# Optimization experiments

Measured on AMD Instinct MI355X. Metric: run time of the kernel, lower is better.

## Reference

```python
import jax, jax.numpy as jnp
import numpy as np

B, T, C, H = 2, 2048, 1024, 16
D = C // H
SCALE = D ** -0.5


def setup_inputs() -> dict:
    key = jax.random.key(0)
    ks = jax.random.split(key, 13)
    s = 0.02
    return {
        "hidden_states": jax.random.normal(ks[0], (B, T, C), dtype=jnp.float32),
        "Wq": jax.random.normal(ks[1], (C, C), dtype=jnp.float32) * s,
        "bq": jax.random.normal(ks[2], (C,), dtype=jnp.float32) * s,
        "Wk": jax.random.normal(ks[3], (C, C), dtype=jnp.float32) * s,
        "bk": jax.random.normal(ks[4], (C,), dtype=jnp.float32) * s,
        "Wv": jax.random.normal(ks[5], (C, C), dtype=jnp.float32) * s,
        "bv": jax.random.normal(ks[6], (C,), dtype=jnp.float32) * s,
        "Wo": jax.random.normal(ks[7], (C, C), dtype=jnp.float32) * s,
        "bo": jax.random.normal(ks[8], (C,), dtype=jnp.float32) * s,
        "Wr1": jax.random.normal(ks[9], (C, C), dtype=jnp.float32) * s,
        "br1": jax.random.normal(ks[10], (C,), dtype=jnp.float32) * s,
        "Wr2": jax.random.normal(ks[11], (C, 3), dtype=jnp.float32) * s,
        "br2": jax.random.normal(ks[12], (3,), dtype=jnp.float32) * s,
    }


def _heads(x):  # [B,T,C] -> [B,H,T,D]
    return x.reshape(B, T, H, D).transpose(0, 2, 1, 3)


def reference(hidden_states, Wq, bq, Wk, bk, Wv, bv, Wo, bo, Wr1, br1, Wr2, br2):
    x = hidden_states
    q = _heads(x @ Wq + bq)  # [B,H,T,D]

    # three memory levels: full sequence, mean-pooled (broadcast), all-zero
    L1 = x
    L2 = jnp.broadcast_to(jnp.mean(x, axis=1, keepdims=True), (B, T, C))
    L3 = jnp.zeros_like(x)

    # soft routing gate per token over the 3 levels
    routing = jax.nn.softmax(jnp.tanh(x @ Wr1 + br1) @ Wr2 + br2, axis=-1)  # [B,T,3]

    out = jnp.zeros_like(x)
    for i, mem in enumerate((L1, L2, L3)):
        k = _heads(mem @ Wk + bk)  # [B,H,T,D]
        v = _heads(mem @ Wv + bv)
        scores = jnp.einsum('bhqd,bhkd->bhqk', q, k) * SCALE
        probs = jax.nn.softmax(scores, axis=-1)
        mo = jnp.einsum('bhqk,bhkd->bhqd', probs, v)  # [B,H,T,D]
        mo = mo.transpose(0, 2, 1, 3).reshape(B, T, C) @ Wo + bo
        out = out + routing[:, :, i:i + 1] * mo
    return out
```

## Files before the change

### kernel.cpp

```cpp
#include <hip/hip_runtime.h>
#include <hip/hip_bf16.h>
#include <math.h>

#define Bdim 2
#define Tdim 2048
#define Cdim 1024
#define Hdim 16
#define SCALE 0.125f
#define M_TOT (Bdim * Tdim)
#define Kdim Cdim
#define KVB 64

typedef __attribute__((ext_vector_type(8))) short bf16x8;
typedef __attribute__((ext_vector_type(4))) float f32x4;
typedef unsigned short ushort_t;

union U8 { bf16x8 v; ushort4 u4[2]; };

__device__ __forceinline__ unsigned short f2bf(float f) {
    union { float f; unsigned u; } v; v.f = f;
    unsigned r = (v.u + 0x7FFFu + ((v.u >> 16) & 1u)) >> 16;
    return (unsigned short)r;
}
__device__ __forceinline__ float bf2f(unsigned short h) {
    union { unsigned u; float f; } v; v.u = ((unsigned)h) << 16;
    return v.f;
}

template <int CTRL>
__device__ __forceinline__ float dppf(float v) {
    int r = __builtin_amdgcn_update_dpp(0, __builtin_bit_cast(int, v), CTRL, 0xF, 0xF, false);
    return __builtin_bit_cast(float, r);
}
__device__ __forceinline__ float rmax16(float v) {
    v = fmaxf(v, dppf<0xB1>(v));
    v = fmaxf(v, dppf<0x4E>(v));
    v = fmaxf(v, dppf<0x124>(v));
    v = fmaxf(v, dppf<0x128>(v));
    return v;
}
__device__ __forceinline__ float rsum16(float v) {
    v += dppf<0xB1>(v);
    v += dppf<0x4E>(v);
    v += dppf<0x124>(v);
    v += dppf<0x128>(v);
    return v;
}

__global__ void colmean_kernel(const float* __restrict__ x, float* __restrict__ m) {
    int b = blockIdx.x;
    int c = blockIdx.y * 256 + threadIdx.x;
    int t0 = blockIdx.z * 64;
    float s = 0.f;
    for (int t = t0; t < t0 + 64; ++t)
        s += x[((size_t)b * Tdim + t) * Cdim + c];
    atomicAdd(&m[b * Cdim + c], s * (1.0f / Tdim));
}

__global__ void biasinit_kernel(const float* __restrict__ bias, float* __restrict__ out, int R) {
    int c = blockIdx.x * 256 + threadIdx.x;
    for (int r = 0; r < R; ++r) out[(size_t)r * Cdim + c] = bias[c];
}

__global__ void gemv3_part_kernel(const float* __restrict__ rows, const float* __restrict__ W,
                                  float* __restrict__ out) {
    int c = blockIdx.x * 256 + threadIdx.x;
    int r = blockIdx.y;
    int k0 = blockIdx.z * 128;
    const float* rp = rows + (size_t)r * Cdim;
    float s = 0.f;
    for (int k = k0; k < k0 + 128; ++k)
        s += rp[k] * W[(size_t)k * Cdim + c];
    atomicAdd(&out[(size_t)r * Cdim + c], s);
}

__global__ void cast_bf16_kernel(const float* __restrict__ in, ushort_t* __restrict__ out) {
    int i = blockIdx.x * 256 + threadIdx.x;
    float4 v = ((const float4*)in)[i];
    ushort4 o;
    o.x = f2bf(v.x); o.y = f2bf(v.y); o.z = f2bf(v.z); o.w = f2bf(v.w);
    ((ushort4*)out)[i] = o;
}

__global__ __launch_bounds__(256) void transpose_cast_kernel(const float* __restrict__ W,
                                                             ushort_t* __restrict__ Wt) {
    __shared__ float L[64][65];
    int n0 = blockIdx.x * 64, k0 = blockIdx.y * 64;
    int t = threadIdx.x;
    int c4 = (t & 15) * 4, rr = t >> 4;
#pragma unroll
    for (int i = 0; i < 4; ++i) {
        int k = rr + i * 16;
        float4 v = *(const float4*)(W + (size_t)(k0 + k) * Cdim + n0 + c4);
        L[k][c4 + 0] = v.x; L[k][c4 + 1] = v.y; L[k][c4 + 2] = v.z; L[k][c4 + 3] = v.w;
    }
    __syncthreads();
#pragma unroll
    for (int i = 0; i < 4; ++i) {
        int n = rr + i * 16;
        ushort4 o;
        o.x = f2bf(L[c4 + 0][n]); o.y = f2bf(L[c4 + 1][n]);
        o.z = f2bf(L[c4 + 2][n]); o.w = f2bf(L[c4 + 3][n]);
        *(ushort4*)(Wt + (size_t)(n0 + n) * Kdim + k0 + c4) = o;
    }
}

__global__ __launch_bounds__(256) void transpose_v_kernel(const ushort_t* __restrict__ Vb,
                                                          ushort_t* __restrict__ Vt) {
    __shared__ ushort_t L[64][72];
    int bh = blockIdx.x, tt = blockIdx.y;
    int b = bh >> 4, h = bh & 15;
    int t = threadIdx.x;
    int tx = t & 15, ty = t >> 4;
#pragma unroll
    for (int it = 0; it < 4; ++it) {
        int tok = ty + it * 16;
        ushort4 v = *(const ushort4*)(Vb + ((size_t)(b * Tdim + tt * 64 + tok)) * Cdim + h * 64 + tx * 4);
        *(ushort4*)&L[tok][tx * 4] = v;
    }
    __syncthreads();
#pragma unroll
    for (int it = 0; it < 4; ++it) {
        int d = ty + it * 16;
        ushort4 o;
        o.x = L[tx * 4 + 0][d]; o.y = L[tx * 4 + 1][d];
        o.z = L[tx * 4 + 2][d]; o.w = L[tx * 4 + 3][d];
        *(ushort4*)(Vt + ((size_t)(bh * 64 + d)) * Tdim + tt * 64 + tx * 4) = o;
    }
}

__device__ __forceinline__ void stage_tile(const ushort_t* __restrict__ A,
                                           const ushort_t* __restrict__ Bt,
                                           ushort_t* ldsbuf, int m0, int n0, int kel,
                                           int wid, int lane) {
#pragma unroll
    for (int i = 0; i < 2; ++i) {
        int c = wid * 128 + i * 64 + lane;
        int row = c >> 3;
        int gch = (c & 7) ^ ((c >> 4) & 7);
        const ushort_t* g = A + (size_t)(m0 + row) * Kdim + kel + gch * 8;
        __builtin_amdgcn_global_load_lds(
            (const __attribute__((address_space(1))) unsigned int*)g,
            (__attribute__((address_space(3))) unsigned int*)(ldsbuf + (wid * 128 + i * 64) * 8),
            16, 0, 0);
    }
#pragma unroll
    for (int i = 0; i < 4; ++i) {
        int c = wid * 256 + i * 64 + lane;
        int row = c >> 3;
        int gch = (c & 7) ^ ((c >> 4) & 7);
        const ushort_t* g = Bt + (size_t)(n0 + row) * Kdim + kel + gch * 8;
        __builtin_amdgcn_global_load_lds(
            (const __attribute__((address_space(1))) unsigned int*)g,
            (__attribute__((address_space(3))) unsigned int*)(ldsbuf + 4096 + (wid * 256 + i * 64) * 8),
            16, 0, 0);
    }
}

template <int MODE>
__global__ __launch_bounds__(256) void gemm_bf16(
    const ushort_t* __restrict__ A, const ushort_t* __restrict__ Bt,
    const float* __restrict__ bias, void* __restrict__ Cout,
    const float* __restrict__ routing, const float* __restrict__ cvec) {
    __shared__ ushort_t lds[2 * 12288];

    int tid = threadIdx.x, lane = tid & 63, wid = tid >> 6;
    int wm = wid >> 1, wn = wid & 1;
    int m0 = blockIdx.y * 64, n0 = blockIdx.x * 128;

    f32x4 acc[2][4];
    f32x4 z = {0.f, 0.f, 0.f, 0.f};
#pragma unroll
    for (int mi = 0; mi < 2; ++mi)
#pragma unroll
        for (int ni = 0; ni < 4; ++ni) acc[mi][ni] = z;

    stage_tile(A, Bt, lds, m0, n0, 0, wid, lane);
    __syncthreads();

    int cur = 0;
    for (int t = 0; t < 16; ++t) {
        if (t < 15) stage_tile(A, Bt, lds + (cur ^ 1) * 12288, m0, n0, (t + 1) * 64, wid, lane);
        const ushort_t* Ab = lds + cur * 12288;
        const ushort_t* Bb = Ab + 4096;
#pragma unroll
        for (int s = 0; s < 2; ++s) {
            int kc = (lane >> 4) + s * 4;
            bf16x8 af[2], bfr[4];
#pragma unroll
            for (int mi = 0; mi < 2; ++mi) {
                int row = wm * 32 + mi * 16 + (lane & 15);
                int ch = kc ^ ((row >> 1) & 7);
                af[mi] = *(const bf16x8*)(Ab + row * 64 + ch * 8);
            }
#pragma unroll
            for (int ni = 0; ni < 4; ++ni) {
                int row = wn * 64 + ni * 16 + (lane & 15);
                int ch = kc ^ ((row >> 1) & 7);
                bfr[ni] = *(const bf16x8*)(Bb + row * 64 + ch * 8);
            }
#pragma unroll
            for (int mi = 0; mi < 2; ++mi)
#pragma unroll
                for (int ni = 0; ni < 4; ++ni)
                    acc[mi][ni] = __builtin_amdgcn_mfma_f32_16x16x32_bf16(
                        af[mi], bfr[ni], acc[mi][ni], 0, 0, 0);
        }
        __syncthreads();
        cur ^= 1;
    }

#pragma unroll
    for (int mi = 0; mi < 2; ++mi)
#pragma unroll
        for (int ni = 0; ni < 4; ++ni) {
            int col = n0 + wn * 64 + ni * 16 + (lane & 15);
            float bs = bias[col];
#pragma unroll
            for (int q = 0; q < 4; ++q) {
                int row = m0 + wm * 32 + mi * 16 + (lane >> 4) * 4 + q;
                float v = acc[mi][ni][q] + bs;
                if constexpr (MODE == 0) {
                    ((ushort_t*)Cout)[(size_t)row * Cdim + col] = f2bf(v);
                } else if constexpr (MODE == 1) {
                    ((float*)Cout)[(size_t)row * Cdim + col] = tanhf(v);
                } else {
                    int b = row >> 11;
                    float r0 = routing[row * 3 + 0];
                    float r1 = routing[row * 3 + 1];
                    float r2 = routing[row * 3 + 2];
                    ((float*)Cout)[(size_t)row * Cdim + col] =
                        r0 * v + r1 * cvec[b * Cdim + col] + r2 * cvec[2 * Cdim + col];
                }
            }
        }
}

__global__ __launch_bounds__(256) void routing_kernel(
    const float* __restrict__ R1, const float* __restrict__ Wr2,
    const float* __restrict__ br2, float* __restrict__ routing) {
    int wid = threadIdx.x >> 6, lane = threadIdx.x & 63;
    int row = blockIdx.x * 4 + wid;
    const float* rp = R1 + (size_t)row * Cdim;
    float a0 = 0.f, a1 = 0.f, a2 = 0.f;
    for (int k = lane; k < Cdim; k += 64) {
        float xv = rp[k];
        a0 += xv * Wr2[k * 3 + 0];
        a1 += xv * Wr2[k * 3 + 1];
        a2 += xv * Wr2[k * 3 + 2];
    }
#pragma unroll
    for (int off = 32; off; off >>= 1) {
        a0 += __shfl_xor(a0, off);
        a1 += __shfl_xor(a1, off);
        a2 += __shfl_xor(a2, off);
    }
    if (lane == 0) {
        a0 += br2[0]; a1 += br2[1]; a2 += br2[2];
        float mx = fmaxf(a0, fmaxf(a1, a2));
        float e0 = __expf(a0 - mx), e1 = __expf(a1 - mx), e2 = __expf(a2 - mx);
        float inv = 1.0f / (e0 + e1 + e2);
        routing[row * 3 + 0] = e0 * inv;
        routing[row * 3 + 1] = e1 * inv;
        routing[row * 3 + 2] = e2 * inv;
    }
}

__global__ __launch_bounds__(256) void flash_mfma(
    const ushort_t* __restrict__ Qg, const ushort_t* __restrict__ Kg,
    const ushort_t* __restrict__ Vtg, ushort_t* __restrict__ MO) {
    __shared__ ushort_t KVs[2][2][64 * 64];
    __shared__ ushort_t Ps[4][32 * 68];

    int tid = threadIdx.x, lane = tid & 63, wid = tid >> 6;
    int tx = lane & 15, g = lane >> 4;
    int bh = blockIdx.x, b = bh >> 4, h = bh & 15;
    int qt = blockIdx.y;

    bf16x8 qf[2][2];
#pragma unroll
    for (int mi = 0; mi < 2; ++mi)
#pragma unroll
        for (int s = 0; s < 2; ++s) {
            int row = qt * 128 + wid * 32 + mi * 16 + tx;
            qf[mi][s] = *(const bf16x8*)(Qg + ((size_t)(b * Tdim + row)) * Cdim + h * 64 + s * 32 + g * 8);
        }

    f32x4 accO[2][4];
    f32x4 z = {0.f, 0.f, 0.f, 0.f};
    float m_run[2][4], l_run[2][4];
#pragma unroll
    for (int mi = 0; mi < 2; ++mi) {
#pragma unroll
        for (int df = 0; df < 4; ++df) accO[mi][df] = z;
#pragma unroll
        for (int q = 0; q < 4; ++q) { m_run[mi][q] = -1e30f; l_run[mi][q] = 0.f; }
    }

    auto stage = [&](int buf, int kt) {
#pragma unroll
        for (int i = 0; i < 2; ++i) {
            int c = wid * 128 + i * 64 + lane;
            int row = c >> 3;
            int gch = (c & 7) ^ ((row >> 1) & 7);
            const ushort_t* gk = Kg + ((size_t)(b * Tdim + kt * KVB + row)) * Cdim + h * 64 + gch * 8;
            __builtin_amdgcn_global_load_lds(
                (const __attribute__((address_space(1))) unsigned int*)gk,
                (__attribute__((address_space(3))) unsigned int*)(&KVs[buf][0][0] + (wid * 128 + i * 64) * 8),
                16, 0, 0);
            const ushort_t* gv = Vtg + ((size_t)(bh * 64 + row)) * Tdim + kt * KVB + gch * 8;
            __builtin_amdgcn_global_load_lds(
                (const __attribute__((address_space(1))) unsigned int*)gv,
                (__attribute__((address_space(3))) unsigned int*)(&KVs[buf][1][0] + (wid * 128 + i * 64) * 8),
                16, 0, 0);
        }
    };

    stage(0, 0);
    __syncthreads();

    for (int kt = 0; kt < Tdim / KVB; ++kt) {
        int buf = kt & 1;
        if (kt < Tdim / KVB - 1) stage(buf ^ 1, kt + 1);
        const ushort_t* Ks = &KVs[buf][0][0];
        const ushort_t* Vs = &KVs[buf][1][0];

        f32x4 sa[2][4];
#pragma unroll
        for (int mi = 0; mi < 2; ++mi)
#pragma unroll
            for (int nf = 0; nf < 4; ++nf) sa[mi][nf] = z;
#pragma unroll
        for (int s = 0; s < 2; ++s)
#pragma unroll
            for (int nf = 0; nf < 4; ++nf) {
                int row = nf * 16 + tx;
                int ch = (g + s * 4) ^ ((row >> 1) & 7);
                bf16x8 kf = *(const bf16x8*)(Ks + row * 64 + ch * 8);
#pragma unroll
                for (int mi = 0; mi < 2; ++mi)
                    sa[mi][nf] = __builtin_amdgcn_mfma_f32_16x16x32_bf16(qf[mi][s], kf, sa[mi][nf], 0, 0, 0);
            }

#pragma unroll
        for (int mi = 0; mi < 2; ++mi) {
#pragma unroll
            for (int q = 0; q < 4; ++q) {
                float mx = fmaxf(fmaxf(sa[mi][0][q], sa[mi][1][q]),
                                 fmaxf(sa[mi][2][q], sa[mi][3][q])) * SCALE;
                mx = rmax16(mx);
                float mold = m_run[mi][q];
                float mnew = fmaxf(mold, mx);
                float corr = __expf(mold - mnew);
                m_run[mi][q] = mnew;
                float psum = 0.f;
#pragma unroll
                for (int nf = 0; nf < 4; ++nf) {
                    float p = __expf(fmaf(sa[mi][nf][q], SCALE, -mnew));
                    Ps[wid][(mi * 16 + g * 4 + q) * 68 + nf * 16 + tx] = f2bf(p);
                    psum += p;
                }
                psum = rsum16(psum);
                l_run[mi][q] = l_run[mi][q] * corr + psum;
#pragma unroll
                for (int df = 0; df < 4; ++df) accO[mi][df][q] *= corr;
            }
        }

#pragma unroll
        for (int s2 = 0; s2 < 2; ++s2) {
            U8 pa[2];
#pragma unroll
            for (int mi = 0; mi < 2; ++mi) {
                const ushort_t* pp = &Ps[wid][(mi * 16 + tx) * 68 + s2 * 32 + g * 8];
                pa[mi].u4[0] = *(const ushort4*)pp;
                pa[mi].u4[1] = *(const ushort4*)(pp + 4);
            }
#pragma unroll
            for (int df = 0; df < 4; ++df) {
                int row = df * 16 + tx;
                int ch = (g + s2 * 4) ^ ((row >> 1) & 7);
                bf16x8 vf = *(const bf16x8*)(Vs + row * 64 + ch * 8);
#pragma unroll
                for (int mi = 0; mi < 2; ++mi)
                    accO[mi][df] = __builtin_amdgcn_mfma_f32_16x16x32_bf16(pa[mi].v, vf, accO[mi][df], 0, 0, 0);
            }
        }
        __syncthreads();
    }

#pragma unroll
    for (int mi = 0; mi < 2; ++mi)
#pragma unroll
        for (int q = 0; q < 4; ++q) {
            float inv = 1.0f / l_run[mi][q];
            int row = qt * 128 + wid * 32 + mi * 16 + g * 4 + q;
#pragma unroll
            for (int df = 0; df < 4; ++df)
                MO[((size_t)(b * Tdim + row)) * Cdim + h * 64 + df * 16 + tx] =
                    f2bf(accO[mi][df][q] * inv);
        }
}

extern "C" void kernel_launch(void* const* d_in, const int* in_sizes, int n_in,
                              void* d_out, int out_size, void* d_ws, size_t ws_size,
                              hipStream_t stream) {
    const float* x   = (const float*)d_in[0];
    const float* Wq  = (const float*)d_in[1];
    const float* bq  = (const float*)d_in[2];
    const float* Wk  = (const float*)d_in[3];
    const float* bk  = (const float*)d_in[4];
    const float* Wv  = (const float*)d_in[5];
    const float* bv  = (const float*)d_in[6];
    const float* Wo  = (const float*)d_in[7];
    const float* bo  = (const float*)d_in[8];
    const float* Wr1 = (const float*)d_in[9];
    const float* br1 = (const float*)d_in[10];
    const float* Wr2 = (const float*)d_in[11];
    const float* br2 = (const float*)d_in[12];
    float* out = (float*)d_out;
    float* ws = (float*)d_ws;

    const size_t MF = 1024 * 1024;
    ushort_t* Qb  = (ushort_t*)ws;
    ushort_t* Kb  = (ushort_t*)(ws + 2 * MF);
    ushort_t* Vb  = (ushort_t*)(ws + 4 * MF);
    float*    R1b = ws + 6 * MF;
    ushort_t* Vtg = (ushort_t*)(ws + 6 * MF);
    ushort_t* MOb = (ushort_t*)(ws + 8 * MF);
    ushort_t* xb  = (ushort_t*)(ws + 10 * MF);
    ushort_t* Wqt  = (ushort_t*)(ws + 12 * MF);
    ushort_t* Wkt  = (ushort_t*)(ws + 12 * MF + 512 * 1024);
    ushort_t* Wvt  = (ushort_t*)(ws + 13 * MF);
    ushort_t* Wr1t = (ushort_t*)(ws + 13 * MF + 512 * 1024);
    ushort_t* Wot  = (ushort_t*)(ws + 14 * MF);
    float* routing = ws + 14 * MF + 512 * 1024;
    float* mvec = routing + 12288;
    float* tmp2 = mvec + 2048;
    float* cvec = tmp2 + 3072;

    hipMemsetAsync(mvec, 0, 2048 * sizeof(float), stream);
    colmean_kernel<<<dim3(Bdim, Cdim / 256, 32), 256, 0, stream>>>(x, mvec);
    biasinit_kernel<<<Cdim / 256, 256, 0, stream>>>(bv, tmp2, 3);
    gemv3_part_kernel<<<dim3(Cdim / 256, 2, 8), 256, 0, stream>>>(mvec, Wv, tmp2);
    biasinit_kernel<<<Cdim / 256, 256, 0, stream>>>(bo, cvec, 3);
    gemv3_part_kernel<<<dim3(Cdim / 256, 3, 8), 256, 0, stream>>>(tmp2, Wo, cvec);

    cast_bf16_kernel<<<4096, 256, 0, stream>>>(x, xb);
    dim3 tg(16, 16);
    transpose_cast_kernel<<<tg, 256, 0, stream>>>(Wq, Wqt);
    transpose_cast_kernel<<<tg, 256, 0, stream>>>(Wk, Wkt);
    transpose_cast_kernel<<<tg, 256, 0, stream>>>(Wv, Wvt);
    transpose_cast_kernel<<<tg, 256, 0, stream>>>(Wr1, Wr1t);
    transpose_cast_kernel<<<tg, 256, 0, stream>>>(Wo, Wot);

    dim3 gg(Cdim / 128, M_TOT / 64);
    gemm_bf16<0><<<gg, 256, 0, stream>>>(xb, Wqt, bq, Qb, nullptr, nullptr);
    gemm_bf16<0><<<gg, 256, 0, stream>>>(xb, Wkt, bk, Kb, nullptr, nullptr);
    gemm_bf16<0><<<gg, 256, 0, stream>>>(xb, Wvt, bv, Vb, nullptr, nullptr);
    gemm_bf16<1><<<gg, 256, 0, stream>>>(xb, Wr1t, br1, R1b, nullptr, nullptr);

    routing_kernel<<<M_TOT / 4, 256, 0, stream>>>(R1b, Wr2, br2, routing);

    transpose_v_kernel<<<dim3(Bdim * Hdim, Tdim / 64), 256, 0, stream>>>(Vb, Vtg);

    flash_mfma<<<dim3(Bdim * Hdim, Tdim / 128), 256, 0, stream>>>(Qb, Kb, Vtg, MOb);

    gemm_bf16<2><<<gg, 256, 0, stream>>>(MOb, Wot, bo, (void*)out, routing, cvec);
}
```

Measured before the change: 326.0 us.

## Fuse QKV/router GEMMs, batch weight transposes, and lazily rescale flash softmax

Merges the five weight transpose-casts into one launch writing a contiguous buffer, and fuses the Q, K, V and router GEMMs into a single 128x128-tile, 512-thread GEMM over the concatenated weights. The flash attention kernel now uses 64-row query tiles with one 16-row fragment per wave, doubling the grid. It also skips the online-softmax rescale unless the running max grows by more than a threshold. These changes cut launch count and improve occupancy and parallelism. The threshold trick lets unnormalised exponentials reach about e^5.5, which stays within bf16/fp32 range but slightly changes numerics.

Measured after the change: 318.9 us. -2.2%, faster.

```diff
diff --git a/kernel.cpp b/kernel.cpp
--- a/kernel.cpp
+++ b/kernel.cpp
@@ -10,6 +10,7 @@
 #define M_TOT (Bdim * Tdim)
 #define Kdim Cdim
 #define KVB 64
+#define THR 5.5f
 
 typedef __attribute__((ext_vector_type(8))) short bf16x8;
 typedef __attribute__((ext_vector_type(4))) float f32x4;
@@ -21,10 +22,6 @@
     union { float f; unsigned u; } v; v.f = f;
     unsigned r = (v.u + 0x7FFFu + ((v.u >> 16) & 1u)) >> 16;
     return (unsigned short)r;
-}
-__device__ __forceinline__ float bf2f(unsigned short h) {
-    union { unsigned u; float f; } v; v.u = ((unsigned)h) << 16;
-    return v.f;
 }
 
 template <int CTRL>
@@ -82,9 +79,14 @@
     ((ushort4*)out)[i] = o;
 }
 
-__global__ __launch_bounds__(256) void transpose_cast_kernel(const float* __restrict__ W,
-                                                             ushort_t* __restrict__ Wt) {
+__global__ __launch_bounds__(256) void transpose_cast5_kernel(
+    const float* __restrict__ W0, const float* __restrict__ W1,
+    const float* __restrict__ W2, const float* __restrict__ W3,
+    const float* __restrict__ W4, ushort_t* __restrict__ Wall) {
     __shared__ float L[64][65];
+    int z = blockIdx.z;
+    const float* W = z == 0 ? W0 : z == 1 ? W1 : z == 2 ? W2 : z == 3 ? W3 : W4;
+    ushort_t* Wt = Wall + (size_t)z * 1024 * 1024;
     int n0 = blockIdx.x * 64, k0 = blockIdx.y * 64;
     int t = threadIdx.x;
     int c4 = (t & 15) * 4, rr = t >> 4;
@@ -129,80 +131,77 @@
     }
 }
 
-__device__ __forceinline__ void stage_tile(const ushort_t* __restrict__ A,
-                                           const ushort_t* __restrict__ Bt,
-                                           ushort_t* ldsbuf, int m0, int n0, int kel,
-                                           int wid, int lane) {
+__device__ __forceinline__ void stage128(const ushort_t* __restrict__ A,
+                                         const ushort_t* __restrict__ Bt,
+                                         ushort_t* ldsbuf, int m0, int n0, int kel,
+                                         int wid, int lane) {
 #pragma unroll
     for (int i = 0; i < 2; ++i) {
         int c = wid * 128 + i * 64 + lane;
         int row = c >> 3;
         int gch = (c & 7) ^ ((c >> 4) & 7);
-        const ushort_t* g = A + (size_t)(m0 + row) * Kdim + kel + gch * 8;
+        const ushort_t* ga = A + (size_t)(m0 + row) * Kdim + kel + gch * 8;
         __builtin_amdgcn_global_load_lds(
-            (const __attribute__((address_space(1))) unsigned int*)g,
+            (const __attribute__((address_space(1))) unsigned int*)ga,
             (__attribute__((address_space(3))) unsigned int*)(ldsbuf + (wid * 128 + i * 64) * 8),
             16, 0, 0);
-    }
-#pragma unroll
-    for (int i = 0; i < 4; ++i) {
-        int c = wid * 256 + i * 64 + lane;
-        int row = c >> 3;
-        int gch = (c & 7) ^ ((c >> 4) & 7);
-        const ushort_t* g = Bt + (size_t)(n0 + row) * Kdim + kel + gch * 8;
+        const ushort_t* gb = Bt + (size_t)(n0 + row) * Kdim + kel + gch * 8;
         __builtin_amdgcn_global_load_lds(
-            (const __attribute__((address_space(1))) unsigned int*)g,
-            (__attribute__((address_space(3))) unsigned int*)(ldsbuf + 4096 + (wid * 256 + i * 64) * 8),
+            (const __attribute__((address_space(1))) unsigned int*)gb,
+            (__attribute__((address_space(3))) unsigned int*)(ldsbuf + 8192 + (wid * 128 + i * 64) * 8),
             16, 0, 0);
     }
 }
 
 template <int MODE>
-__global__ __launch_bounds__(256) void gemm_bf16(
+__global__ __launch_bounds__(512) void gemm128(
     const ushort_t* __restrict__ A, const ushort_t* __restrict__ Bt,
-    const float* __restrict__ bias, void* __restrict__ Cout,
-    const float* __restrict__ routing, const float* __restrict__ cvec) {
-    __shared__ ushort_t lds[2 * 12288];
+    const float* __restrict__ b0, const float* __restrict__ b1,
+    const float* __restrict__ b2, const float* __restrict__ b3,
+    ushort_t* __restrict__ oQ, ushort_t* __restrict__ oK, ushort_t* __restrict__ oV,
+    float* __restrict__ oF, const float* __restrict__ routing, const float* __restrict__ cvec) {
+    __shared__ ushort_t lds[2 * 16384];
 
     int tid = threadIdx.x, lane = tid & 63, wid = tid >> 6;
-    int wm = wid >> 1, wn = wid & 1;
-    int m0 = blockIdx.y * 64, n0 = blockIdx.x * 128;
-
-    f32x4 acc[2][4];
+    int tx = lane & 15, g = lane >> 4;
+    int wm = wid >> 2, wn = wid & 3;
+    int m0 = blockIdx.y * 128, n0 = blockIdx.x * 128;
+
+    f32x4 acc[4][2];
     f32x4 z = {0.f, 0.f, 0.f, 0.f};
 #pragma unroll
-    for (int mi = 0; mi < 2; ++mi)
-#pragma unroll
-        for (int ni = 0; ni < 4; ++ni) acc[mi][ni] = z;
-
-    stage_tile(A, Bt, lds, m0, n0, 0, wid, lane);
+    for (int mi = 0; mi < 4; ++mi)
+#pragma unroll
+        for (int ni = 0; ni < 2; ++ni) acc[mi][ni] = z;
+
+    stage128(A, Bt, lds, m0, n0, 0, wid, lane);
     __syncthreads();
 
     int cur = 0;
     for (int t = 0; t < 16; ++t) {
-        if (t < 15) stage_tile(A, Bt, lds + (cur ^ 1) * 12288, m0, n0, (t + 1) * 64, wid, lane);
-        const ushort_t* Ab = lds + cur * 12288;
-        const ushort_t* Bb = Ab + 4096;
+        if (t < 15) stage128(A, Bt, lds + (cur ^ 1) * 16384, m0, n0, (t + 1) * 64, wid, lane);
+        const ushort_t* Ab = lds + cur * 16384;
+        const ushort_t* Bb = Ab + 8192;
 #pragma unroll
         for (int s = 0; s < 2; ++s) {
-            int kc = (lane >> 4) + s * 4;
-            bf16x8 af[2], bfr[4];
-#pragma unroll
-            for (int mi = 0; mi < 2; ++mi) {
-                int row = wm * 32 + mi * 16 + (lane & 15);
+            int kc = g + s * 4;
+            bf16x8 af[4], bfr[2];
+#pragma unroll
+            for (int mi = 0; mi < 4; ++mi) {
+                int row = wm * 64 + mi * 16 + tx;
                 int ch = kc ^ ((row >> 1) & 7);
                 af[mi] = *(const bf16x8*)(Ab + row * 64 + ch * 8);
             }
 #pragma unroll
-            for (int ni = 0; ni < 4; ++ni) {
-                int row = wn * 64 + ni * 16 + (lane & 15);
+            for (int ni = 0; ni < 2; ++ni) {
+                int row = wn * 32 + ni * 16 + tx;
                 int ch = kc ^ ((row >> 1) & 7);
                 bfr[ni] = *(const bf16x8*)(Bb + row * 64 + ch * 8);
             }
 #pragma unroll
-            for (int mi = 0; mi < 2; ++mi)
-#pragma unroll
-                for (int ni = 0; ni < 4; ++ni)
+            for (int mi = 0; mi < 4; ++mi)
+#pragma unroll
+                for (int ni = 0; ni < 2; ++ni)
                     acc[mi][ni] = __builtin_amdgcn_mfma_f32_16x16x32_bf16(
                         af[mi], bfr[ni], acc[mi][ni], 0, 0, 0);
         }
@@ -210,30 +209,47 @@
         cur ^= 1;
     }
 
-#pragma unroll
-    for (int mi = 0; mi < 2; ++mi)
-#pragma unroll
-        for (int ni = 0; ni < 4; ++ni) {
-            int col = n0 + wn * 64 + ni * 16 + (lane & 15);
-            float bs = bias[col];
-#pragma unroll
-            for (int q = 0; q < 4; ++q) {
-                int row = m0 + wm * 32 + mi * 16 + (lane >> 4) * 4 + q;
-                float v = acc[mi][ni][q] + bs;
-                if constexpr (MODE == 0) {
-                    ((ushort_t*)Cout)[(size_t)row * Cdim + col] = f2bf(v);
-                } else if constexpr (MODE == 1) {
-                    ((float*)Cout)[(size_t)row * Cdim + col] = tanhf(v);
-                } else {
+    if constexpr (MODE == 3) {
+        int w = n0 >> 10;
+        const float* bias = w == 0 ? b0 : w == 1 ? b1 : w == 2 ? b2 : b3;
+        ushort_t* obf = w == 0 ? oQ : w == 1 ? oK : oV;
+        int nloc = n0 & 1023;
+#pragma unroll
+        for (int mi = 0; mi < 4; ++mi)
+#pragma unroll
+            for (int ni = 0; ni < 2; ++ni) {
+                int col = nloc + wn * 32 + ni * 16 + tx;
+                float bs = bias[col];
+#pragma unroll
+                for (int q = 0; q < 4; ++q) {
+                    int row = m0 + wm * 64 + mi * 16 + g * 4 + q;
+                    float v = acc[mi][ni][q] + bs;
+                    if (w == 3)
+                        oF[(size_t)row * Cdim + col] = tanhf(v);
+                    else
+                        obf[(size_t)row * Cdim + col] = f2bf(v);
+                }
+            }
+    } else {
+#pragma unroll
+        for (int mi = 0; mi < 4; ++mi)
+#pragma unroll
+            for (int ni = 0; ni < 2; ++ni) {
+                int col = n0 + wn * 32 + ni * 16 + tx;
+                float bs = b0[col];
+#pragma unroll
+                for (int q = 0; q < 4; ++q) {
+                    int row = m0 + wm * 64 + mi * 16 + g * 4 + q;
+                    float v = acc[mi][ni][q] + bs;
                     int b = row >> 11;
                     float r0 = routing[row * 3 + 0];
                     float r1 = routing[row * 3 + 1];
                     float r2 = routing[row * 3 + 2];
-                    ((float*)Cout)[(size_t)row * Cdim + col] =
+                    oF[(size_t)row * Cdim + col] =
                         r0 * v + r1 * cvec[b * Cdim + col] + r2 * cvec[2 * Cdim + col];
                 }
             }
-        }
+    }
 }
 
 __global__ __launch_bounds__(256) void routing_kernel(
@@ -270,32 +286,27 @@
     const ushort_t* __restrict__ Qg, const ushort_t* __restrict__ Kg,
     const ushort_t* __restrict__ Vtg, ushort_t* __restrict__ MO) {
     __shared__ ushort_t KVs[2][2][64 * 64];
-    __shared__ ushort_t Ps[4][32 * 68];
+    __shared__ ushort_t Ps[4][16 * 68];
 
     int tid = threadIdx.x, lane = tid & 63, wid = tid >> 6;
     int tx = lane & 15, g = lane >> 4;
     int bh = blockIdx.x, b = bh >> 4, h = bh & 15;
     int qt = blockIdx.y;
 
-    bf16x8 qf[2][2];
-#pragma unroll
-    for (int mi = 0; mi < 2; ++mi)
-#pragma unroll
-        for (int s = 0; s < 2; ++s) {
-            int row = qt * 128 + wid * 32 + mi * 16 + tx;
-            qf[mi][s] = *(const bf16x8*)(Qg + ((size_t)(b * Tdim + row)) * Cdim + h * 64 + s * 32 + g * 8);
-        }
-
-    f32x4 accO[2][4];
+    bf16x8 qf[2];
+#pragma unroll
+    for (int s = 0; s < 2; ++s) {
+        int row = qt * 64 + wid * 16 + tx;
+        qf[s] = *(const bf16x8*)(Qg + ((size_t)(b * Tdim + row)) * Cdim + h * 64 + s * 32 + g * 8);
+    }
+
+    f32x4 accO[4];
     f32x4 z = {0.f, 0.f, 0.f, 0.f};
-    float m_run[2][4], l_run[2][4];
-#pragma unroll
-    for (int mi = 0; mi < 2; ++mi) {
-#pragma unroll
-        for (int df = 0; df < 4; ++df) accO[mi][df] = z;
-#pragma unroll
-        for (int q = 0; q < 4; ++q) { m_run[mi][q] = -1e30f; l_run[mi][q] = 0.f; }
-    }
+    float m_run[4], l_run[4];
+#pragma unroll
+    for (int df = 0; df < 4; ++df) accO[df] = z;
+#pragma unroll
+    for (int q = 0; q < 4; ++q) { m_run[q] = -3e38f; l_run[q] = 0.f; }
 
     auto stage = [&](int buf, int kt) {
 #pragma unroll
@@ -325,11 +336,9 @@
         const ushort_t* Ks = &KVs[buf][0][0];
         const ushort_t* Vs = &KVs[buf][1][0];
 
-        f32x4 sa[2][4];
-#pragma unroll
-        for (int mi = 0; mi < 2; ++mi)
-#pragma unroll
-            for (int nf = 0; nf < 4; ++nf) sa[mi][nf] = z;
+        f32x4 sa[4];
+#pragma unroll
+        for (int nf = 0; nf < 4; ++nf) sa[nf] = z;
 #pragma unroll
         for (int s = 0; s < 2; ++s)
 #pragma unroll
@@ -337,69 +346,67 @@
                 int row = nf * 16 + tx;
                 int ch = (g + s * 4) ^ ((row >> 1) & 7);
                 bf16x8 kf = *(const bf16x8*)(Ks + row * 64 + ch * 8);
-#pragma unroll
-                for (int mi = 0; mi < 2; ++mi)
-                    sa[mi][nf] = __builtin_amdgcn_mfma_f32_16x16x32_bf16(qf[mi][s], kf, sa[mi][nf], 0, 0, 0);
-            }
-
-#pragma unroll
-        for (int mi = 0; mi < 2; ++mi) {
+                sa[nf] = __builtin_amdgcn_mfma_f32_16x16x32_bf16(qf[s], kf, sa[nf], 0, 0, 0);
+            }
+
+        float pmax[4];
+        int need = 0;
+#pragma unroll
+        for (int q = 0; q < 4; ++q) {
+            float mx = fmaxf(fmaxf(sa[0][q], sa[1][q]), fmaxf(sa[2][q], sa[3][q]));
+            pmax[q] = rmax16(mx) * SCALE;
+            need |= (pmax[q] > m_run[q] + THR);
+        }
+        if (__any(need)) {
 #pragma unroll
             for (int q = 0; q < 4; ++q) {
-                float mx = fmaxf(fmaxf(sa[mi][0][q], sa[mi][1][q]),
-                                 fmaxf(sa[mi][2][q], sa[mi][3][q])) * SCALE;
-                mx = rmax16(mx);
-                float mold = m_run[mi][q];
-                float mnew = fmaxf(mold, mx);
-                float corr = __expf(mold - mnew);
-                m_run[mi][q] = mnew;
-                float psum = 0.f;
-#pragma unroll
-                for (int nf = 0; nf < 4; ++nf) {
-                    float p = __expf(fmaf(sa[mi][nf][q], SCALE, -mnew));
-                    Ps[wid][(mi * 16 + g * 4 + q) * 68 + nf * 16 + tx] = f2bf(p);
-                    psum += p;
-                }
-                psum = rsum16(psum);
-                l_run[mi][q] = l_run[mi][q] * corr + psum;
-#pragma unroll
-                for (int df = 0; df < 4; ++df) accO[mi][df][q] *= corr;
-            }
+                float mnew = fmaxf(m_run[q], pmax[q]);
+                float corr = __expf(m_run[q] - mnew);
+                l_run[q] *= corr;
+#pragma unroll
+                for (int df = 0; df < 4; ++df) accO[df][q] *= corr;
+                m_run[q] = mnew;
+            }
+        }
+
+#pragma unroll
+        for (int q = 0; q < 4; ++q) {
+            float psum = 0.f;
+#pragma unroll
+            for (int nf = 0; nf < 4; ++nf) {
+                float p = __expf(fmaf(sa[nf][q], SCALE, -m_run[q]));
+                Ps[wid][(g * 4 + q) * 68 + nf * 16 + tx] = f2bf(p);
+                psum += p;
+            }
+            l_run[q] += rsum16(psum);
         }
 
 #pragma unroll
         for (int s2 = 0; s2 < 2; ++s2) {
-            U8 pa[2];
-#pragma unroll
-            for (int mi = 0; mi < 2; ++mi) {
-                const ushort_t* pp = &Ps[wid][(mi * 16 + tx) * 68 + s2 * 32 + g * 8];
-                pa[mi].u4[0] = *(const ushort4*)pp;
-                pa[mi].u4[1] = *(const ushort4*)(pp + 4);
-            }
+            U8 pa;
+            const ushort_t* pp = &Ps[wid][tx * 68 + s2 * 32 + g * 8];
+            pa.u4[0] = *(const ushort4*)pp;
+            pa.u4[1] = *(const ushort4*)(pp + 4);
 #pragma unroll
             for (int df = 0; df < 4; ++df) {
                 int row = df * 16 + tx;
                 int ch = (g + s2 * 4) ^ ((row >> 1) & 7);
                 bf16x8 vf = *(const bf16x8*)(Vs + row * 64 + ch * 8);
-#pragma unroll
-                for (int mi = 0; mi < 2; ++mi)
-                    accO[mi][df] = __builtin_amdgcn_mfma_f32_16x16x32_bf16(pa[mi].v, vf, accO[mi][df], 0, 0, 0);
+                accO[df] = __builtin_amdgcn_mfma_f32_16x16x32_bf16(pa.v, vf, accO[df], 0, 0, 0);
             }
         }
         __syncthreads();
     }
 
 #pragma unroll
-    for (int mi = 0; mi < 2; ++mi)
-#pragma unroll
-        for (int q = 0; q < 4; ++q) {
-            float inv = 1.0f / l_run[mi][q];
-            int row = qt * 128 + wid * 32 + mi * 16 + g * 4 + q;
-#pragma unroll
-            for (int df = 0; df < 4; ++df)
-                MO[((size_t)(b * Tdim + row)) * Cdim + h * 64 + df * 16 + tx] =
-                    f2bf(accO[mi][df][q] * inv);
-        }
+    for (int q = 0; q < 4; ++q) {
+        float inv = 1.0f / l_run[q];
+        int row = qt * 64 + wid * 16 + g * 4 + q;
+#pragma unroll
+        for (int df = 0; df < 4; ++df)
+            MO[((size_t)(b * Tdim + row)) * Cdim + h * 64 + df * 16 + tx] =
+                f2bf(accO[df][q] * inv);
+    }
 }
 
 extern "C" void kernel_launch(void* const* d_in, const int* in_sizes, int n_in,
@@ -422,18 +429,14 @@
     float* ws = (float*)d_ws;
 
     const size_t MF = 1024 * 1024;
-    ushort_t* Qb  = (ushort_t*)ws;
-    ushort_t* Kb  = (ushort_t*)(ws + 2 * MF);
-    ushort_t* Vb  = (ushort_t*)(ws + 4 * MF);
-    float*    R1b = ws + 6 * MF;
-    ushort_t* Vtg = (ushort_t*)(ws + 6 * MF);
-    ushort_t* MOb = (ushort_t*)(ws + 8 * MF);
-    ushort_t* xb  = (ushort_t*)(ws + 10 * MF);
-    ushort_t* Wqt  = (ushort_t*)(ws + 12 * MF);
-    ushort_t* Wkt  = (ushort_t*)(ws + 12 * MF + 512 * 1024);
-    ushort_t* Wvt  = (ushort_t*)(ws + 13 * MF);
-    ushort_t* Wr1t = (ushort_t*)(ws + 13 * MF + 512 * 1024);
-    ushort_t* Wot  = (ushort_t*)(ws + 14 * MF);
+    ushort_t* Qb   = (ushort_t*)ws;
+    ushort_t* Kb   = (ushort_t*)(ws + 2 * MF);
+    ushort_t* Vb   = (ushort_t*)(ws + 4 * MF);
+    float*    R1b  = ws + 6 * MF;
+    ushort_t* Vtg  = (ushort_t*)(ws + 6 * MF);
+    ushort_t* MOb  = (ushort_t*)(ws + 8 * MF);
+    ushort_t* xb   = (ushort_t*)(ws + 10 * MF);
+    ushort_t* Wall = (ushort_t*)(ws + 12 * MF);
     float* routing = ws + 14 * MF + 512 * 1024;
     float* mvec = routing + 12288;
     float* tmp2 = mvec + 2048;
@@ -447,24 +450,19 @@
     gemv3_part_kernel<<<dim3(Cdim / 256, 3, 8), 256, 0, stream>>>(tmp2, Wo, cvec);
 
     cast_bf16_kernel<<<4096, 256, 0, stream>>>(x, xb);
-    dim3 tg(16, 16);
-    transpose_cast_kernel<<<tg, 256, 0, stream>>>(Wq, Wqt);
-    transpose_cast_kernel<<<tg, 256, 0, stream>>>(Wk, Wkt);
-    transpose_cast_kernel<<<tg, 256, 0, stream>>>(Wv, Wvt);
-    transpose_cast_kernel<<<tg, 256, 0, stream>>>(Wr1, Wr1t);
-    transpose_cast_kernel<<<tg, 256, 0, stream>>>(Wo, Wot);
-
-    dim3 gg(Cdim / 128, M_TOT / 64);
-    gemm_bf16<0><<<gg, 256, 0, stream>>>(xb, Wqt, bq, Qb, nullptr, nullptr);
-    gemm_bf16<0><<<gg, 256, 0, stream>>>(xb, Wkt, bk, Kb, nullptr, nullptr);
-    gemm_bf16<0><<<gg, 256, 0, stream>>>(xb, Wvt, bv, Vb, nullptr, nullptr);
-    gemm_bf16<1><<<gg, 256, 0, stream>>>(xb, Wr1t, br1, R1b, nullptr, nullptr);
+    transpose_cast5_kernel<<<dim3(16, 16, 5), 256, 0, stream>>>(Wq, Wk, Wv, Wr1, Wo, Wall);
+
+    gemm128<3><<<dim3(32, 32), 512, 0, stream>>>(xb, Wall, bq, bk, bv, br1,
+                                                 Qb, Kb, Vb, R1b, nullptr, nullptr);
 
     routing_kernel<<<M_TOT / 4, 256, 0, stream>>>(R1b, Wr2, br2, routing);
 
     transpose_v_kernel<<<dim3(Bdim * Hdim, Tdim / 64), 256, 0, stream>>>(Vb, Vtg);
 
-    flash_mfma<<<dim3(Bdim * Hdim, Tdim / 128), 256, 0, stream>>>(Qb, Kb, Vtg, MOb);
-
-    gemm_bf16<2><<<gg, 256, 0, stream>>>(MOb, Wot, bo, (void*)out, routing, cvec);
-}
+    flash_mfma<<<dim3(Bdim * Hdim, Tdim / 64), 256, 0, stream>>>(Qb, Kb, Vtg, MOb);
+
+    gemm128<2><<<dim3(8, 32), 512, 0, stream>>>(MOb, Wall + (size_t)4 * 1024 * 1024,
+                                                bo, nullptr, nullptr, nullptr,
+                                                nullptr, nullptr, nullptr,
+                                                out, routing, cvec);
+}
```
